# Optimization experiments

Measured on AMD Instinct MI355X. Metric: run time of the kernel, lower is better.

Reference implementation:

```python
import jax, jax.numpy as jnp
import numpy as np

D_MODEL = 512
NUM_HEADS = 8
D_K = D_MODEL // NUM_HEADS


def setup_inputs() -> dict:
    key = jax.random.key(0)
    k0, k1, k2, k3, k4 = jax.random.split(key, 5)
    s = 1.0 / np.sqrt(D_MODEL)
    return {
        "x": jax.random.normal(k0, (2, 4096, D_MODEL), dtype=jnp.float32),
        "W_q": jax.random.normal(k1, (D_MODEL, D_MODEL), dtype=jnp.float32) * s,
        "W_k": jax.random.normal(k2, (D_MODEL, D_MODEL), dtype=jnp.float32) * s,
        "W_v": jax.random.normal(k3, (D_MODEL, D_MODEL), dtype=jnp.float32) * s,
        "W_o": jax.random.normal(k4, (D_MODEL, D_MODEL), dtype=jnp.float32) * s,
    }


def reference(x, W_q, W_k, W_v, W_o):
    B, S, _ = x.shape
    # project and split heads: (B, H, S, d_k)
    def split(t):
        return t.reshape(B, S, NUM_HEADS, D_K).transpose(0, 2, 1, 3)
    Q = split(x @ W_q)
    K = split(x @ W_k)
    V = split(x @ W_v)
    scale = jnp.sqrt(jnp.asarray(D_K, dtype=x.dtype))
    logits = jnp.einsum('bhqd,bhkd->bhqk', Q, K) / scale
    attn = jax.nn.softmax(logits, axis=-1)  # dropout is identity at inference
    out = jnp.einsum('bhqk,bhkd->bhqd', attn, V)
    concat = out.transpose(0, 2, 1, 3).reshape(B, S, D_MODEL)
    return concat @ W_o
```

## Files before the change

kernel.cpp:

```cpp
#include <hip/hip_runtime.h>
#include <hip/hip_bf16.h>


#define DMODEL 512
#define SEQ    4096
#define NTOK   8192
#define LDQK   1024

using f32x4 = __attribute__((ext_vector_type(4))) float;
using s16x8 = __attribute__((ext_vector_type(8))) short;
using u16x8 = __attribute__((ext_vector_type(8))) unsigned short;

static __device__ __forceinline__ unsigned short f2bf(float f) {
  union { float f; unsigned u; } v; v.f = f;
  unsigned r = v.u + 0x7fff + ((v.u >> 16) & 1);
  return (unsigned short)(r >> 16);
}

static __device__ __forceinline__ unsigned pack_bf2(float lo, float hi) {
  __hip_bfloat162 t = __float22bfloat162_rn(make_float2(lo, hi));
  union { __hip_bfloat162 b; unsigned u; } c; c.b = t; return c.u;
}

static __device__ __forceinline__ void gll16(const void* g, void* l) {
  __builtin_amdgcn_global_load_lds(
      (const __attribute__((address_space(1))) unsigned int*)g,
      (__attribute__((address_space(3))) unsigned int*)l, 16, 0, 0);
}

__global__ void cast_x_kernel(const float* __restrict__ x,
                              unsigned short* __restrict__ xb, int n4) {
  int i = blockIdx.x * blockDim.x + threadIdx.x;
  if (i >= n4) return;
  float4 v = ((const float4*)x)[i];
  ushort4 o;
  o.x = f2bf(v.x); o.y = f2bf(v.y); o.z = f2bf(v.z); o.w = f2bf(v.w);
  ((ushort4*)xb)[i] = o;
}

__global__ void wtrans4_kernel(const float* __restrict__ Wq,
                               const float* __restrict__ Wk,
                               const float* __restrict__ Wv,
                               const float* __restrict__ Wo,
                               unsigned short* __restrict__ Wall, float c2) {
  __shared__ float T[64][65];
  const int y = blockIdx.y;
  const float* W = (y == 0) ? Wq : (y == 1) ? Wk : (y == 2) ? Wv : Wo;
  const float scale = (y == 0) ? c2 : 1.0f;
  const int tk = (blockIdx.x & 7) * 64;
  const int tn = (blockIdx.x >> 3) * 64;
  const int r  = threadIdx.x >> 2;
  const int cq = threadIdx.x & 3;
#pragma unroll
  for (int i = 0; i < 4; ++i) {
    int c = (cq + 4 * i) * 4;
    float4 v = *(const float4*)&W[(size_t)(tk + r) * 512 + tn + c];
    T[r][c + 0] = v.x * scale; T[r][c + 1] = v.y * scale;
    T[r][c + 2] = v.z * scale; T[r][c + 3] = v.w * scale;
  }
  __syncthreads();
  const int n  = threadIdx.x >> 2;
  const int k0 = (threadIdx.x & 3) * 16;
#pragma unroll
  for (int j4 = 0; j4 < 4; ++j4) {
    ushort4 o;
    o.x = f2bf(T[k0 + j4 * 4 + 0][n]);
    o.y = f2bf(T[k0 + j4 * 4 + 1][n]);
    o.z = f2bf(T[k0 + j4 * 4 + 2][n]);
    o.w = f2bf(T[k0 + j4 * 4 + 3][n]);
    *(ushort4*)&Wall[(size_t)y * 262144 + (size_t)(tn + n) * 512 + tk + k0 + j4 * 4] = o;
  }
}

__global__ __launch_bounds__(256, 3) void gemm_qkv(
    const unsigned short* __restrict__ xb,
    const unsigned short* __restrict__ Wall,
    unsigned short* __restrict__ QKb,
    unsigned short* __restrict__ Vtb)
{
  __shared__ unsigned short As[128 * 32];
  __shared__ unsigned short Bs[128 * 32];
  const int by = blockIdx.y;
  const bool vmode = (by >= 8);
  const unsigned short* A  = vmode ? (Wall + 2 * 262144) : xb;
  const unsigned short* Bt = vmode ? xb : Wall;
  const size_t bm = vmode ? (size_t)(by - 8) * 128 : (size_t)blockIdx.x * 128;
  const size_t bn = vmode ? (size_t)blockIdx.x * 128 : (size_t)by * 128;
  const int tid  = threadIdx.x;
  const int wave = tid >> 6, lane = tid & 63;
  const int q4 = lane >> 4, ln = lane & 15;
  const int wm = (wave >> 1) * 64, wn = (wave & 1) * 64;
  f32x4 acc[4][4] = {};
  const int srow = wave * 16 + (lane >> 2);
  const int scol = (lane & 3) * 8;

  const unsigned short* Ag  = A  + (bm + srow)      * 512 + scol;
  const unsigned short* Ag2 = A  + (bm + 64 + srow) * 512 + scol;
  const unsigned short* Bg  = Bt + (bn + srow)      * 512 + scol;
  const unsigned short* Bg2 = Bt + (bn + 64 + srow) * 512 + scol;
  unsigned short* Ad  = As + wave * 512;
  unsigned short* Ad2 = As + 2048 + wave * 512;
  unsigned short* Bd  = Bs + wave * 512;
  unsigned short* Bd2 = Bs + 2048 + wave * 512;

  for (int kt = 0; kt < 512; kt += 32) {
    __syncthreads();
    gll16(Ag + kt,  Ad);
    gll16(Ag2 + kt, Ad2);
    gll16(Bg + kt,  Bd);
    gll16(Bg2 + kt, Bd2);
    __syncthreads();
    s16x8 af[4], bfr[4];
#pragma unroll
    for (int i = 0; i < 4; i++)
      af[i] = *(const s16x8*)(As + (wm + i * 16 + ln) * 32 + q4 * 8);
#pragma unroll
    for (int i = 0; i < 4; i++)
      bfr[i] = *(const s16x8*)(Bs + (wn + i * 16 + ln) * 32 + q4 * 8);
#pragma unroll
    for (int mi = 0; mi < 4; mi++)
#pragma unroll
      for (int ni = 0; ni < 4; ni++)
        acc[mi][ni] = __builtin_amdgcn_mfma_f32_16x16x32_bf16(
            af[mi], bfr[ni], acc[mi][ni], 0, 0, 0);
  }
#pragma unroll
  for (int mi = 0; mi < 4; mi++)
#pragma unroll
    for (int r = 0; r < 4; ++r) {
      size_t row = bm + wm + mi * 16 + q4 * 4 + r;
#pragma unroll
      for (int ni = 0; ni < 4; ni++) {
        size_t col = bn + wn + ni * 16 + ln;
        unsigned short hv = f2bf(acc[mi][ni][r]);
        if (!vmode) {
          QKb[row * 1024 + col] = hv;
        } else {
          int b = (int)(col >> 12), s = (int)(col & 4095);
          int sp = (s & ~63) | (s & 32) | (((s >> 2) & 3) << 3) |
                   (((s >> 4) & 1) << 2) | (s & 3);
          Vtb[(size_t)b * 2097152 + row * 4096 + sp] = hv;
        }
      }
    }
}

__global__ __launch_bounds__(256, 2) void attn_kernel(
    const unsigned short* __restrict__ QK,
    const unsigned short* __restrict__ Vt,
    unsigned short* __restrict__ Oc)
{
  const int qt = blockIdx.x, h = blockIdx.y, b = blockIdx.z;
  const int tid = threadIdx.x, wave = tid >> 6, lane = tid & 63;
  const int q4 = lane >> 4, ln = lane & 15;
  const int wq = wave >> 1, wk = wave & 1;
  __shared__ __align__(16) unsigned char SM[36864];
  unsigned short* KsB = (unsigned short*)SM;
  unsigned short* VsB = (unsigned short*)(SM + 18432);
  const size_t rowbase = (size_t)b * SEQ;
  const size_t qrow0   = (size_t)qt * 128 + wq * 64;
  const unsigned short* Kp  = QK + rowbase * LDQK + 512 + h * 64;
  const unsigned short* VTp = Vt + ((size_t)(b * 8 + h) * 64) * SEQ;

  s16x8 qf[4][2];
#pragma unroll
  for (int nt = 0; nt < 4; ++nt) {
    const unsigned short* q = QK + (rowbase + qrow0 + nt * 16 + ln) * LDQK + h * 64;
    qf[nt][0] = *(const s16x8*)(q + q4 * 8);
    qf[nt][1] = *(const s16x8*)(q + 32 + q4 * 8);
  }
  f32x4 o[4][4] = {};
  float lp[4] = {};

  const int srow = tid >> 2;
  const int scol = (tid & 3) * 16;

  const unsigned short* kgp = Kp  + (size_t)srow * LDQK + scol;
  const unsigned short* vgp = VTp + (size_t)srow * SEQ  + scol;

  u16x8 kr  = *(const u16x8*)kgp;
  u16x8 kr2 = *(const u16x8*)(kgp + 8);
  u16x8 vr  = *(const u16x8*)vgp;
  u16x8 vr2 = *(const u16x8*)(vgp + 8);
  *(u16x8*)(KsB + srow * 72 + scol)     = kr;
  *(u16x8*)(KsB + srow * 72 + scol + 8) = kr2;
  *(u16x8*)(VsB + srow * 72 + scol)     = vr;
  *(u16x8*)(VsB + srow * 72 + scol + 8) = vr2;
  kgp += (size_t)64 * LDQK;  vgp += 64;
  kr  = *(const u16x8*)kgp;
  kr2 = *(const u16x8*)(kgp + 8);
  vr  = *(const u16x8*)vgp;
  vr2 = *(const u16x8*)(vgp + 8);
  __syncthreads();

  for (int t = 0; t < SEQ / 64; ++t) {
    const int cur = t & 1;
    const unsigned short* Kc = KsB + cur * 4608;
    const unsigned short* Vc = VsB + cur * 4608;

    f32x4 s4[2][4] = {};
#pragma unroll
    for (int mi = 0; mi < 2; ++mi)
#pragma unroll
      for (int c = 0; c < 2; ++c) {
        s16x8 kf = *(const s16x8*)(Kc + (wk * 32 + mi * 16 + ln) * 72 + c * 32 + q4 * 8);
#pragma unroll
        for (int nt = 0; nt < 4; ++nt)
          s4[mi][nt] = __builtin_amdgcn_mfma_f32_16x16x32_bf16(kf, qf[nt][c], s4[mi][nt], 0, 0, 0);
      }
    s16x8 vf[4];
#pragma unroll
    for (int dt = 0; dt < 4; ++dt)
      vf[dt] = *(const s16x8*)(Vc + (dt * 16 + ln) * 72 + wk * 32 + q4 * 8);

    s16x8 pf[4];
#pragma unroll
    for (int nt = 0; nt < 4; ++nt) {
      float e00 = __builtin_amdgcn_exp2f(s4[0][nt][0]);
      float e01 = __builtin_amdgcn_exp2f(s4[0][nt][1]);
      float e02 = __builtin_amdgcn_exp2f(s4[0][nt][2]);
      float e03 = __builtin_amdgcn_exp2f(s4[0][nt][3]);
      float e10 = __builtin_amdgcn_exp2f(s4[1][nt][0]);
      float e11 = __builtin_amdgcn_exp2f(s4[1][nt][1]);
      float e12 = __builtin_amdgcn_exp2f(s4[1][nt][2]);
      float e13 = __builtin_amdgcn_exp2f(s4[1][nt][3]);
      lp[nt] += ((e00 + e01) + (e02 + e03)) + ((e10 + e11) + (e12 + e13));
      union { s16x8 v; unsigned u[4]; } pu;
      pu.u[0] = pack_bf2(e00, e01);
      pu.u[1] = pack_bf2(e02, e03);
      pu.u[2] = pack_bf2(e10, e11);
      pu.u[3] = pack_bf2(e12, e13);
      pf[nt] = pu.v;
    }
#pragma unroll
    for (int nt = 0; nt < 4; ++nt)
#pragma unroll
      for (int dt = 0; dt < 4; ++dt)
        o[nt][dt] = __builtin_amdgcn_mfma_f32_16x16x32_bf16(pf[nt], vf[dt], o[nt][dt], 0, 0, 0);

    if (t + 1 < SEQ / 64) {
      unsigned short* Kn = KsB + (cur ^ 1) * 4608;
      unsigned short* Vn = VsB + (cur ^ 1) * 4608;
      *(u16x8*)(Kn + srow * 72 + scol)     = kr;
      *(u16x8*)(Kn + srow * 72 + scol + 8) = kr2;
      *(u16x8*)(Vn + srow * 72 + scol)     = vr;
      *(u16x8*)(Vn + srow * 72 + scol + 8) = vr2;
      if (t + 2 < SEQ / 64) {
        kgp += (size_t)64 * LDQK;  vgp += 64;
        kr  = *(const u16x8*)kgp;
        kr2 = *(const u16x8*)(kgp + 8);
        vr  = *(const u16x8*)vgp;
        vr2 = *(const u16x8*)(vgp + 8);
      }
    }
    __syncthreads();
  }

#pragma unroll
  for (int nt = 0; nt < 4; ++nt) {
    lp[nt] += __shfl_xor(lp[nt], 16, 64);
    lp[nt] += __shfl_xor(lp[nt], 32, 64);
  }
  float* Red  = (float*)SM;
  float* RedL = (float*)(SM + 32768);
  if (wk == 1) {
#pragma unroll
    for (int nt = 0; nt < 4; ++nt) {
#pragma unroll
      for (int dt = 0; dt < 4; ++dt)
        *(f32x4*)(Red + ((wq * 16 + nt * 4 + dt) * 64 + lane) * 4) = o[nt][dt];
      RedL[(wq * 4 + nt) * 64 + lane] = lp[nt];
    }
  }
  __syncthreads();
  if (wk == 0) {
#pragma unroll
    for (int nt = 0; nt < 4; ++nt) {
#pragma unroll
      for (int dt = 0; dt < 4; ++dt)
        o[nt][dt] += *(const f32x4*)(Red + ((wq * 16 + nt * 4 + dt) * 64 + lane) * 4);
      lp[nt] += RedL[(wq * 4 + nt) * 64 + lane];
    }
#pragma unroll
    for (int nt = 0; nt < 4; ++nt)
#pragma unroll
      for (int r = 0; r < 4; ++r) {
        float lv = __shfl(lp[nt], q4 * 4 + r, 64);
        float inv = 1.0f / lv;
        size_t row = rowbase + qrow0 + nt * 16 + q4 * 4 + r;
#pragma unroll
        for (int dt = 0; dt < 4; ++dt)
          Oc[row * DMODEL + h * 64 + dt * 16 + ln] = f2bf(o[nt][dt][r] * inv);
      }
  }
}

__global__ __launch_bounds__(256, 3) void gemm_out(
    const unsigned short* __restrict__ A,
    const unsigned short* __restrict__ Bt,
    float* __restrict__ C)
{
  __shared__ unsigned short As[128 * 32];
  __shared__ unsigned short Bs[64 * 32];
  const int tid  = threadIdx.x;
  const int wave = tid >> 6, lane = tid & 63;
  const int q4 = lane >> 4, ln = lane & 15;
  const size_t bm = (size_t)blockIdx.x * 128;
  const size_t bn = (size_t)blockIdx.y * 64;
  const int wm = (wave >> 1) * 64, wn = (wave & 1) * 32;
  f32x4 acc[4][2] = {};
  const int srow = wave * 16 + (lane >> 2);
  const int scol = (lane & 3) * 8;

  const unsigned short* Ag  = A  + (bm + srow)      * 512 + scol;
  const unsigned short* Ag2 = A  + (bm + 64 + srow) * 512 + scol;
  const unsigned short* Bg  = Bt + (bn + srow)      * 512 + scol;
  unsigned short* Ad  = As + wave * 512;
  unsigned short* Ad2 = As + 2048 + wave * 512;
  unsigned short* Bd  = Bs + wave * 512;

  for (int kt = 0; kt < 512; kt += 32) {
    __syncthreads();
    gll16(Ag + kt,  Ad);
    gll16(Ag2 + kt, Ad2);
    gll16(Bg + kt,  Bd);
    __syncthreads();
    s16x8 af[4], bfr[2];
#pragma unroll
    for (int i = 0; i < 4; i++)
      af[i] = *(const s16x8*)(As + (wm + i * 16 + ln) * 32 + q4 * 8);
#pragma unroll
    for (int i = 0; i < 2; i++)
      bfr[i] = *(const s16x8*)(Bs + (wn + i * 16 + ln) * 32 + q4 * 8);
#pragma unroll
    for (int mi = 0; mi < 4; mi++)
#pragma unroll
      for (int ni = 0; ni < 2; ni++)
        acc[mi][ni] = __builtin_amdgcn_mfma_f32_16x16x32_bf16(
            af[mi], bfr[ni], acc[mi][ni], 0, 0, 0);
  }
#pragma unroll
  for (int mi = 0; mi < 4; mi++)
#pragma unroll
    for (int r = 0; r < 4; ++r) {
      size_t row = bm + wm + mi * 16 + q4 * 4 + r;
#pragma unroll
      for (int ni = 0; ni < 2; ni++)
        C[row * 512 + bn + wn + ni * 16 + ln] = acc[mi][ni][r];
    }
}

extern "C" void kernel_launch(void* const* d_in, const int* in_sizes, int n_in,
                              void* d_out, int out_size, void* d_ws, size_t ws_size,
                              hipStream_t stream) {
  const float* x  = (const float*)d_in[0];
  const float* Wq = (const float*)d_in[1];
  const float* Wk = (const float*)d_in[2];
  const float* Wv = (const float*)d_in[3];
  const float* Wo = (const float*)d_in[4];

  char* ws = (char*)d_ws;
  unsigned short* xb   = (unsigned short*)(ws);
  unsigned short* Wall = (unsigned short*)(ws + 8388608);
  unsigned short* QKb  = (unsigned short*)(ws + 10485760);
  unsigned short* Vtb  = (unsigned short*)(ws + 27262976);
  unsigned short* Oc   = (unsigned short*)(ws + 35651584);

  const float C2 = 0.125f * 1.44269504088896f;

  hipLaunchKernelGGL(cast_x_kernel, dim3(NTOK * DMODEL / 4 / 256), dim3(256), 0,
                     stream, x, xb, NTOK * DMODEL / 4);
  hipLaunchKernelGGL(wtrans4_kernel, dim3(64, 4), dim3(256), 0, stream,
                     Wq, Wk, Wv, Wo, Wall, C2);
  hipLaunchKernelGGL(gemm_qkv, dim3(64, 12), dim3(256), 0, stream,
                     xb, Wall, QKb, Vtb);
  hipLaunchKernelGGL(attn_kernel, dim3(32, 8, 2), dim3(256), 0, stream,
                     QKb, Vtb, Oc);
  hipLaunchKernelGGL(gemm_out, dim3(64, 8), dim3(256), 0, stream,
                     Oc, Wall + 3 * 262144, (float*)d_out);
}
```

Baseline: 192.5 us.

## Split attention over two key chunks with a combine pass; merge prep kernels

The attention kernel now splits each head's key/value sequence into two halves across the z grid dimension. This doubles the block count and raises launch bounds to 4 blocks per CU to improve occupancy. Each half writes unnormalized fp32 partial outputs and row sums to workspace, and a new combine kernel sums them, normalizes, and casts to bf16. The x cast and weight transpose kernels are also merged into one launch to save launch overhead. The trade-off is extra global memory traffic for the fp32 partials, an added launch, and register pressure from the tighter launch bounds.

After: 563.7 us. +192.9%, slower.

```diff
diff --git a/kernel.cpp b/kernel.cpp
--- a/kernel.cpp
+++ b/kernel.cpp
@@ -28,27 +28,30 @@
       (__attribute__((address_space(3))) unsigned int*)l, 16, 0, 0);
 }
 
-__global__ void cast_x_kernel(const float* __restrict__ x,
-                              unsigned short* __restrict__ xb, int n4) {
-  int i = blockIdx.x * blockDim.x + threadIdx.x;
-  if (i >= n4) return;
-  float4 v = ((const float4*)x)[i];
-  ushort4 o;
-  o.x = f2bf(v.x); o.y = f2bf(v.y); o.z = f2bf(v.z); o.w = f2bf(v.w);
-  ((ushort4*)xb)[i] = o;
-}
-
-__global__ void wtrans4_kernel(const float* __restrict__ Wq,
-                               const float* __restrict__ Wk,
-                               const float* __restrict__ Wv,
-                               const float* __restrict__ Wo,
-                               unsigned short* __restrict__ Wall, float c2) {
+__global__ void prep_kernel(const float* __restrict__ x,
+                            const float* __restrict__ Wq,
+                            const float* __restrict__ Wk,
+                            const float* __restrict__ Wv,
+                            const float* __restrict__ Wo,
+                            unsigned short* __restrict__ xb,
+                            unsigned short* __restrict__ Wall, float c2) {
   __shared__ float T[64][65];
-  const int y = blockIdx.y;
+  const int bx = blockIdx.x;
+  if (bx < 1024) {
+    for (int i = bx * 256 + threadIdx.x; i < NTOK * DMODEL / 4; i += 262144) {
+      float4 v = ((const float4*)x)[i];
+      ushort4 o;
+      o.x = f2bf(v.x); o.y = f2bf(v.y); o.z = f2bf(v.z); o.w = f2bf(v.w);
+      ((ushort4*)xb)[i] = o;
+    }
+    return;
+  }
+  const int t = bx - 1024;
+  const int y = t >> 6, sub = t & 63;
   const float* W = (y == 0) ? Wq : (y == 1) ? Wk : (y == 2) ? Wv : Wo;
   const float scale = (y == 0) ? c2 : 1.0f;
-  const int tk = (blockIdx.x & 7) * 64;
-  const int tn = (blockIdx.x >> 3) * 64;
+  const int tk = (sub & 7) * 64;
+  const int tn = (sub >> 3) * 64;
   const int r  = threadIdx.x >> 2;
   const int cq = threadIdx.x & 3;
 #pragma unroll
@@ -145,12 +148,14 @@
     }
 }
 
-__global__ __launch_bounds__(256, 2) void attn_kernel(
+__global__ __launch_bounds__(256, 4) void attn_kernel(
     const unsigned short* __restrict__ QK,
     const unsigned short* __restrict__ Vt,
-    unsigned short* __restrict__ Oc)
+    float* __restrict__ Opart,
+    float* __restrict__ Lpart)
 {
-  const int qt = blockIdx.x, h = blockIdx.y, b = blockIdx.z;
+  const int qt = blockIdx.x, h = blockIdx.y, z = blockIdx.z;
+  const int b = z >> 1, ck = z & 1;
   const int tid = threadIdx.x, wave = tid >> 6, lane = tid & 63;
   const int q4 = lane >> 4, ln = lane & 15;
   const int wq = wave >> 1, wk = wave & 1;
@@ -175,8 +180,8 @@
   const int srow = tid >> 2;
   const int scol = (tid & 3) * 16;
 
-  const unsigned short* kgp = Kp  + (size_t)srow * LDQK + scol;
-  const unsigned short* vgp = VTp + (size_t)srow * SEQ  + scol;
+  const unsigned short* kgp = Kp  + ((size_t)(ck * 2048 + srow)) * LDQK + scol;
+  const unsigned short* vgp = VTp + (size_t)srow * SEQ + ck * 2048 + scol;
 
   u16x8 kr  = *(const u16x8*)kgp;
   u16x8 kr2 = *(const u16x8*)(kgp + 8);
@@ -193,7 +198,7 @@
   vr2 = *(const u16x8*)(vgp + 8);
   __syncthreads();
 
-  for (int t = 0; t < SEQ / 64; ++t) {
+  for (int t = 0; t < 32; ++t) {
     const int cur = t & 1;
     const unsigned short* Kc = KsB + cur * 4608;
     const unsigned short* Vc = VsB + cur * 4608;
@@ -238,14 +243,14 @@
       for (int dt = 0; dt < 4; ++dt)
         o[nt][dt] = __builtin_amdgcn_mfma_f32_16x16x32_bf16(pf[nt], vf[dt], o[nt][dt], 0, 0, 0);
 
-    if (t + 1 < SEQ / 64) {
+    if (t + 1 < 32) {
       unsigned short* Kn = KsB + (cur ^ 1) * 4608;
       unsigned short* Vn = VsB + (cur ^ 1) * 4608;
       *(u16x8*)(Kn + srow * 72 + scol)     = kr;
       *(u16x8*)(Kn + srow * 72 + scol + 8) = kr2;
       *(u16x8*)(Vn + srow * 72 + scol)     = vr;
       *(u16x8*)(Vn + srow * 72 + scol + 8) = vr2;
-      if (t + 2 < SEQ / 64) {
+      if (t + 2 < 32) {
         kgp += (size_t)64 * LDQK;  vgp += 64;
         kr  = *(const u16x8*)kgp;
         kr2 = *(const u16x8*)(kgp + 8);
@@ -274,25 +279,46 @@
   }
   __syncthreads();
   if (wk == 0) {
+    float* Opc = Opart + (size_t)ck * NTOK * DMODEL;
 #pragma unroll
     for (int nt = 0; nt < 4; ++nt) {
 #pragma unroll
       for (int dt = 0; dt < 4; ++dt)
         o[nt][dt] += *(const f32x4*)(Red + ((wq * 16 + nt * 4 + dt) * 64 + lane) * 4);
       lp[nt] += RedL[(wq * 4 + nt) * 64 + lane];
+      if (q4 == 0)
+        Lpart[(size_t)ck * 65536 + (size_t)(b * 8 + h) * 4096 + qrow0 + nt * 16 + ln] = lp[nt];
     }
 #pragma unroll
     for (int nt = 0; nt < 4; ++nt)
 #pragma unroll
       for (int r = 0; r < 4; ++r) {
-        float lv = __shfl(lp[nt], q4 * 4 + r, 64);
-        float inv = 1.0f / lv;
         size_t row = rowbase + qrow0 + nt * 16 + q4 * 4 + r;
 #pragma unroll
         for (int dt = 0; dt < 4; ++dt)
-          Oc[row * DMODEL + h * 64 + dt * 16 + ln] = f2bf(o[nt][dt][r] * inv);
+          Opc[row * DMODEL + h * 64 + dt * 16 + ln] = o[nt][dt][r];
       }
   }
+}
+
+__global__ void combine_kernel(const float* __restrict__ Opart,
+                               const float* __restrict__ Lpart,
+                               unsigned short* __restrict__ Oc) {
+  int i = blockIdx.x * 256 + threadIdx.x;
+  int row = i >> 7;
+  int c4  = (i & 127) * 4;
+  int b = row >> 12, qrow = row & 4095, h = c4 >> 6;
+  float l = Lpart[(size_t)(b * 8 + h) * 4096 + qrow] +
+            Lpart[65536 + (size_t)(b * 8 + h) * 4096 + qrow];
+  float inv = 1.0f / l;
+  f32x4 a = *(const f32x4*)(Opart + (size_t)row * 512 + c4);
+  f32x4 c = *(const f32x4*)(Opart + (size_t)NTOK * DMODEL + (size_t)row * 512 + c4);
+  float r0 = (a[0] + c[0]) * inv, r1 = (a[1] + c[1]) * inv;
+  float r2 = (a[2] + c[2]) * inv, r3 = (a[3] + c[3]) * inv;
+  uint2 w;
+  w.x = pack_bf2(r0, r1);
+  w.y = pack_bf2(r2, r3);
+  *(uint2*)&Oc[(size_t)row * 512 + c4] = w;
 }
 
 __global__ __launch_bounds__(256, 3) void gemm_out(
@@ -360,22 +386,24 @@
   const float* Wo = (const float*)d_in[4];
 
   char* ws = (char*)d_ws;
-  unsigned short* xb   = (unsigned short*)(ws);
-  unsigned short* Wall = (unsigned short*)(ws + 8388608);
-  unsigned short* QKb  = (unsigned short*)(ws + 10485760);
-  unsigned short* Vtb  = (unsigned short*)(ws + 27262976);
-  unsigned short* Oc   = (unsigned short*)(ws + 35651584);
+  unsigned short* xb    = (unsigned short*)(ws);
+  unsigned short* Wall  = (unsigned short*)(ws + 8388608);
+  unsigned short* QKb   = (unsigned short*)(ws + 10485760);
+  unsigned short* Vtb   = (unsigned short*)(ws + 27262976);
+  unsigned short* Oc    = (unsigned short*)(ws + 35651584);
+  float*          Opart = (float*)(ws + 44040192);
+  float*          Lpart = (float*)(ws + 77594624);
 
   const float C2 = 0.125f * 1.44269504088896f;
 
-  hipLaunchKernelGGL(cast_x_kernel, dim3(NTOK * DMODEL / 4 / 256), dim3(256), 0,
-                     stream, x, xb, NTOK * DMODEL / 4);
-  hipLaunchKernelGGL(wtrans4_kernel, dim3(64, 4), dim3(256), 0, stream,
-                     Wq, Wk, Wv, Wo, Wall, C2);
+  hipLaunchKernelGGL(prep_kernel, dim3(1280), dim3(256), 0, stream,
+                     x, Wq, Wk, Wv, Wo, xb, Wall, C2);
   hipLaunchKernelGGL(gemm_qkv, dim3(64, 12), dim3(256), 0, stream,
                      xb, Wall, QKb, Vtb);
-  hipLaunchKernelGGL(attn_kernel, dim3(32, 8, 2), dim3(256), 0, stream,
-                     QKb, Vtb, Oc);
+  hipLaunchKernelGGL(attn_kernel, dim3(32, 8, 4), dim3(256), 0, stream,
+                     QKb, Vtb, Opart, Lpart);
+  hipLaunchKernelGGL(combine_kernel, dim3(4096), dim3(256), 0, stream,
+                     Opart, Lpart, Oc);
   hipLaunchKernelGGL(gemm_out, dim3(64, 8), dim3(256), 0, stream,
                      Oc, Wall + 3 * 262144, (float*)d_out);
 }
```
